# Kernel optimization log

Measured on AMD Instinct MI355X. Metric: run time of the kernel, lower is better.

Reference implementation:

```python
import jax, jax.numpy as jnp
import numpy as np

N = 4096  # input_features == output_features == transform length (power of 2)


def _fft(x, twiddle_factors):
    """Faithful vectorized form of the module's radix-2 butterfly network.

    x: (N, D) complex64. twiddle_factors: (N, D) float32 (the learned weights).
    Original loop: for each stage `step`, for each block, for r in [0, half):
        k = r * (N // step)
        temp = exp(-2j*pi*k/N * twiddle_factors[k]) * x[j + half]
        new x[j + half] = x[j] - temp ; new x[j] = x[j] + temp
    Blocks are independent, so each stage is a single batched butterfly.
    """
    n = x.shape[0]
    # initial permutation: index xor with N//2 (as written in the source; not full bit-reversal)
    x = x[jnp.bitwise_xor(jnp.arange(n), n // 2)]
    step = 2
    while step <= n:  # log2(N) stages, fixed small Python loop
        half = step // 2
        k = jnp.arange(half) * (n // step)                      # (half,)
        phase = (-2.0 * jnp.pi) * (k[:, None].astype(jnp.float32) / n) * twiddle_factors[k]
        tw = jnp.exp(1j * phase)                                # (half, D) complex64
        xr = x.reshape(n // step, step, -1)                     # (blocks, step, D)
        top = xr[:, :half]
        bot = xr[:, half:]
        temp = tw[None] * bot                                   # (blocks, half, D)
        x = jnp.concatenate([top + temp, top - temp], axis=1).reshape(n, -1)
        step *= 2
    return x


def setup_inputs() -> dict:
    key = jax.random.key(0)
    kx, kw = jax.random.split(key)
    x = jax.random.normal(kx, (N, N), dtype=jnp.float32)
    weights = jax.random.normal(kw, (N, N), dtype=jnp.float32)  # nn.Parameter(randn(out, in))
    return {"x": x, "weights": weights}


def reference(x, weights):
    # input_features == output_features -> no pad / no truncation branch taken
    return _fft(x.astype(jnp.complex64), weights)
```

## Files before the change

kernel.cpp:

```cpp
#include <hip/hip_runtime.h>

#define INV_N (1.0f / 4096.0f)

__device__ __forceinline__ void bf(float& ar, float& ai, float& br, float& bi,
                                   float s, float cs) {
    float tr = cs * br - s * bi;
    float ti = cs * bi + s * br;
    br = ar - tr; bi = ai - ti;
    ar = ar + tr; ai = ai + ti;
}

__device__ __forceinline__ void tw(int k, float wk, float* s, float* cs) {
    float rev = (float)k * (-INV_N) * wk;
    rev = __builtin_amdgcn_fractf(rev);
    *s  = __builtin_amdgcn_sinf(rev);
    *cs = __builtin_amdgcn_cosf(rev);
}

__device__ __forceinline__ void exchange(float2* tile, float (&ar)[16],
                                         float (&ai)[16], int pb, int c) {
#pragma unroll
    for (int par = 0; par < 2; ++par) {
#pragma unroll
        for (int m = 0; m < 16; ++m) {
            if (((pb + (m >> 2) + (m & 3)) & 1) == par) {
                int srow = (pb << 3) + (((m >> 2) << 1) | ((m & 3) >> 1));
                tile[srow * 64 + c] = make_float2(ar[m], ai[m]);
            }
        }
        __syncthreads();
#pragma unroll
        for (int m = 0; m < 16; ++m) {
            if (((pb + (m >> 2) + (m & 3)) & 1) == par) {
                int srow = ((m >> 2) << 3) + ((m & 3) << 1) + (pb >> 1);
                float2 v = tile[srow * 64 + c];
                ar[m] = v.x; ai[m] = v.y;
            }
        }
        if (par == 0) __syncthreads();
    }
}

__global__ __launch_bounds__(256) void fft_lo(const float* __restrict__ x,
                                              const float* __restrict__ w,
                                              float2* __restrict__ dst2,
                                              unsigned dst_lim2) {
    __shared__ __align__(16) float2 tile[32 * 64];
    const int t   = threadIdx.x;
    const int c   = t & 63;
    const int pb  = t >> 6;
    const int c0  = (blockIdx.x & 63) << 6;
    const int r0  = (blockIdx.x >> 6) << 6;
    const int src_r0 = r0 ^ 2048;
    const unsigned col = (unsigned)(c0 + c);

    float ar[16], ai[16];
#pragma unroll
    for (int m = 0; m < 16; ++m) {
        unsigned gi = (unsigned)(src_r0 + 16 * pb + m) * 4096u + col;
        ar[m] = __builtin_nontemporal_load(&x[gi]);
        ai[m] = 0.f;
    }

    float wp1[7];
#pragma unroll
    for (int i = 0; i < 7; ++i)
        wp1[i] = w[(unsigned)(256 * (i + 1)) * 4096u + col];

    float w2a[4], w2b[8];
#pragma unroll
    for (int i = 0; i < 4; ++i)
        w2a[i] = w[(unsigned)((pb + 4 * i) * 128) * 4096u + col];
#pragma unroll
    for (int i = 0; i < 8; ++i)
        w2b[i] = w[(unsigned)((pb + 4 * i) * 64) * 4096u + col];

    float s1[8], c1[8];
    s1[0] = 0.f; c1[0] = 1.f;
#pragma unroll
    for (int i = 1; i < 8; ++i)
        tw(256 * i, wp1[i - 1], &s1[i], &c1[i]);

#pragma unroll
    for (int h = 1; h <= 8; h <<= 1) {
        const int step = h << 1;
#pragma unroll
        for (int r = 0; r < h; ++r) {
            const int ti = r * (8 / h);
            const float s = s1[ti], cs = c1[ti];
#pragma unroll
            for (int b = 0; b < 8 / h; ++b) {
                const int mt = b * step + r;
                bf(ar[mt], ai[mt], ar[mt + h], ai[mt + h], s, cs);
            }
        }
    }

    float s2a[4], c2a[4], s2b[8], c2b[8];
#pragma unroll
    for (int i = 0; i < 4; ++i)
        tw((pb + 4 * i) * 128, w2a[i], &s2a[i], &c2a[i]);
#pragma unroll
    for (int i = 0; i < 8; ++i)
        tw((pb + 4 * i) * 64, w2b[i], &s2b[i], &c2b[i]);

    exchange(tile, ar, ai, pb, c);

#pragma unroll
    for (int rm = 0; rm < 4; ++rm) {
#pragma unroll
        for (int b = 0; b < 2; ++b) {
            const int mt = b * 8 + rm;
            bf(ar[mt], ai[mt], ar[mt + 4], ai[mt + 4], s2a[rm], c2a[rm]);
        }
    }
#pragma unroll
    for (int m = 0; m < 8; ++m)
        bf(ar[m], ai[m], ar[m + 8], ai[m + 8], s2b[m], c2b[m]);

#pragma unroll
    for (int m = 0; m < 16; ++m) {
        unsigned gi = (unsigned)(r0 + pb + 4 * m) * 4096u + col;
        if (gi < dst_lim2) dst2[gi] = make_float2(ar[m], ai[m]);
    }
}

template <int REAL_OUT>
__global__ __launch_bounds__(256) void fft_hi(const float* __restrict__ w,
                                              const float2* __restrict__ src2,
                                              float2* __restrict__ dstc,
                                              float* __restrict__ dstr,
                                              unsigned dst_lim) {
    __shared__ __align__(16) float2 tile[32 * 64];
    const int t    = threadIdx.x;
    const int c    = t & 63;
    const int pb   = t >> 6;
    const int rres = blockIdx.x >> 6;
    const unsigned col = (unsigned)(((blockIdx.x & 63) << 6) + c);

    float ar[16], ai[16];
#pragma unroll
    for (int m = 0; m < 16; ++m) {
        unsigned gi = (unsigned)(rres + 64 * (16 * pb + m)) * 4096u + col;
        float2 v = src2[gi];
        ar[m] = v.x; ai[m] = v.y;
    }

    float wp1, wp2[2], wp4[4], wp8[8];
    wp1 = w[(unsigned)(rres * 32) * 4096u + col];
#pragma unroll
    for (int r = 0; r < 2; ++r)
        wp2[r] = w[(unsigned)((rres + 64 * r) * 16) * 4096u + col];
#pragma unroll
    for (int r = 0; r < 4; ++r)
        wp4[r] = w[(unsigned)((rres + 64 * r) * 8) * 4096u + col];
#pragma unroll
    for (int r = 0; r < 8; ++r)
        wp8[r] = w[(unsigned)((rres + 64 * r) * 4) * 4096u + col];

    float w2a[4], w2b[8];
#pragma unroll
    for (int i = 0; i < 4; ++i)
        w2a[i] = w[(unsigned)((rres + 64 * (pb + 4 * i)) * 2) * 4096u + col];
#pragma unroll
    for (int i = 0; i < 8; ++i)
        w2b[i] = w[(unsigned)(rres + 64 * (pb + 4 * i)) * 4096u + col];

    {
        float s, cs;
        tw(rres * 32, wp1, &s, &cs);
#pragma unroll
        for (int b = 0; b < 8; ++b)
            bf(ar[2 * b], ai[2 * b], ar[2 * b + 1], ai[2 * b + 1], s, cs);
    }
#pragma unroll
    for (int r = 0; r < 2; ++r) {
        float s, cs;
        tw((rres + 64 * r) * 16, wp2[r], &s, &cs);
#pragma unroll
        for (int b = 0; b < 4; ++b) {
            const int mt = b * 4 + r;
            bf(ar[mt], ai[mt], ar[mt + 2], ai[mt + 2], s, cs);
        }
    }
#pragma unroll
    for (int r = 0; r < 4; ++r) {
        float s, cs;
        tw((rres + 64 * r) * 8, wp4[r], &s, &cs);
#pragma unroll
        for (int b = 0; b < 2; ++b) {
            const int mt = b * 8 + r;
            bf(ar[mt], ai[mt], ar[mt + 4], ai[mt + 4], s, cs);
        }
    }
#pragma unroll
    for (int r = 0; r < 8; ++r) {
        float s, cs;
        tw((rres + 64 * r) * 4, wp8[r], &s, &cs);
        bf(ar[r], ai[r], ar[r + 8], ai[r + 8], s, cs);
    }

    float s2a[4], c2a[4], s2b[8], c2b[8];
#pragma unroll
    for (int i = 0; i < 4; ++i)
        tw((rres + 64 * (pb + 4 * i)) * 2, w2a[i], &s2a[i], &c2a[i]);
#pragma unroll
    for (int i = 0; i < 8; ++i)
        tw(rres + 64 * (pb + 4 * i), w2b[i], &s2b[i], &c2b[i]);

    exchange(tile, ar, ai, pb, c);

#pragma unroll
    for (int rm = 0; rm < 4; ++rm) {
#pragma unroll
        for (int b = 0; b < 2; ++b) {
            const int mt = b * 8 + rm;
            bf(ar[mt], ai[mt], ar[mt + 4], ai[mt + 4], s2a[rm], c2a[rm]);
        }
    }
#pragma unroll
    for (int m = 0; m < 8; ++m)
        bf(ar[m], ai[m], ar[m + 8], ai[m + 8], s2b[m], c2b[m]);

    if (REAL_OUT) {
#pragma unroll
        for (int m = 0; m < 16; ++m) {
            unsigned gi = (unsigned)(rres + 64 * (pb + 4 * m)) * 4096u + col;
            if (gi < dst_lim) __builtin_nontemporal_store(ar[m], &dstr[gi]);
        }
    } else {
#pragma unroll
        for (int m = 0; m < 16; ++m) {
            unsigned gi = (unsigned)(rres + 64 * (pb + 4 * m)) * 4096u + col;
            if (gi < dst_lim) dstc[gi] = make_float2(ar[m], ai[m]);
        }
    }
}

extern "C" void kernel_launch(void* const* d_in, const int* in_sizes, int n_in,
                              void* d_out, int out_size, void* d_ws, size_t ws_size,
                              hipStream_t stream) {
    const float* x = (const float*)d_in[0];
    const float* w = (const float*)d_in[1];
    const long long NN = 4096LL * 4096LL;

    if ((long long)out_size >= 2 * NN) {
        float2* o2 = (float2*)d_out;
        unsigned lim2 = (unsigned)(out_size / 2);
        fft_lo<<<4096, 256, 0, stream>>>(x, w, o2, lim2);
        fft_hi<0><<<4096, 256, 0, stream>>>(w, o2, o2, nullptr, lim2);
    } else {
        float2* ws2 = (float2*)d_ws;
        unsigned ws_lim2 = (unsigned)(ws_size / 8);
        unsigned out_lim = (unsigned)out_size;
        fft_lo<<<4096, 256, 0, stream>>>(x, w, ws2, ws_lim2);
        fft_hi<1><<<4096, 256, 0, stream>>>(w, (const float2*)ws2, nullptr,
                                            (float*)d_out, out_lim);
    }
}
```

Before: 200.5 us.

## Stage twiddle weights into LDS via async global_load_lds and dedupe loads

Replaces per-thread register loads of the twiddle weights with asynchronous direct-to-LDS loads, spread across the four waves so each weight row is fetched once per block instead of redundantly by every wave. Twiddle computation for the second stage group now runs after the exchange and reads from LDS. Custom barrier macros replace __syncthreads, with explicit vmcnt/lgkmcnt waits. This lowers VGPR pressure and redundant global traffic, but adds LDS use (about 14–16 KB more per block), which may reduce occupancy. Correctness relies on hand-written waitcnt handling.

```diff
diff --git a/kernel.cpp b/kernel.cpp
--- a/kernel.cpp
+++ b/kernel.cpp
@@ -17,6 +17,18 @@
     *cs = __builtin_amdgcn_cosf(rev);
 }
 
+__device__ __forceinline__ void load_lds4(const float* gp, float* lp) {
+    __builtin_amdgcn_global_load_lds(
+        (const __attribute__((address_space(1))) void*)gp,
+        (__attribute__((address_space(3))) void*)lp, 4, 0, 0);
+}
+
+#define BAR() do { asm volatile("s_waitcnt lgkmcnt(0)" ::: "memory"); \
+                   __builtin_amdgcn_s_barrier(); } while (0)
+
+#define STAGE_BAR() do { asm volatile("s_waitcnt vmcnt(0)" ::: "memory"); \
+                         __builtin_amdgcn_s_barrier(); } while (0)
+
 __device__ __forceinline__ void exchange(float2* tile, float (&ar)[16],
                                          float (&ai)[16], int pb, int c) {
 #pragma unroll
@@ -28,7 +40,7 @@
                 tile[srow * 64 + c] = make_float2(ar[m], ai[m]);
             }
         }
-        __syncthreads();
+        BAR();
 #pragma unroll
         for (int m = 0; m < 16; ++m) {
             if (((pb + (m >> 2) + (m & 3)) & 1) == par) {
@@ -37,8 +49,23 @@
                 ar[m] = v.x; ai[m] = v.y;
             }
         }
-        if (par == 0) __syncthreads();
-    }
+        if (par == 0) BAR();
+    }
+}
+
+__device__ __forceinline__ unsigned lo_row(int i) {
+    if (i < 32) return (unsigned)(64 * i);
+    if (i < 48) return (unsigned)((i - 32) * 128);
+    return (unsigned)((i - 47) * 256);
+}
+
+__device__ __forceinline__ unsigned hi_row(int i, int rres) {
+    if (i < 32) return (unsigned)(rres + 64 * i);
+    if (i < 48) return (unsigned)((rres + 64 * (i - 32)) * 2);
+    if (i < 56) return (unsigned)((rres + 64 * (i - 48)) * 4);
+    if (i < 60) return (unsigned)((rres + 64 * (i - 56)) * 8);
+    if (i < 62) return (unsigned)((rres + 64 * (i - 60)) * 16);
+    return (unsigned)(rres * 32);
 }
 
 __global__ __launch_bounds__(256) void fft_lo(const float* __restrict__ x,
@@ -46,14 +73,23 @@
                                               float2* __restrict__ dst2,
                                               unsigned dst_lim2) {
     __shared__ __align__(16) float2 tile[32 * 64];
+    __shared__ __align__(16) float  lds_w[55 * 64];
     const int t   = threadIdx.x;
     const int c   = t & 63;
     const int pb  = t >> 6;
+    const int wv  = t >> 6;
     const int c0  = (blockIdx.x & 63) << 6;
     const int r0  = (blockIdx.x >> 6) << 6;
     const int src_r0 = r0 ^ 2048;
     const unsigned col = (unsigned)(c0 + c);
 
+#pragma unroll
+    for (int ii = 0; ii < 14; ++ii) {
+        int i = 4 * ii + wv;
+        if (i < 55)
+            load_lds4(w + (size_t)lo_row(i) * 4096u + col, lds_w + i * 64);
+    }
+
     float ar[16], ai[16];
 #pragma unroll
     for (int m = 0; m < 16; ++m) {
@@ -62,24 +98,13 @@
         ai[m] = 0.f;
     }
 
-    float wp1[7];
-#pragma unroll
-    for (int i = 0; i < 7; ++i)
-        wp1[i] = w[(unsigned)(256 * (i + 1)) * 4096u + col];
-
-    float w2a[4], w2b[8];
-#pragma unroll
-    for (int i = 0; i < 4; ++i)
-        w2a[i] = w[(unsigned)((pb + 4 * i) * 128) * 4096u + col];
-#pragma unroll
-    for (int i = 0; i < 8; ++i)
-        w2b[i] = w[(unsigned)((pb + 4 * i) * 64) * 4096u + col];
+    STAGE_BAR();
 
     float s1[8], c1[8];
     s1[0] = 0.f; c1[0] = 1.f;
 #pragma unroll
-    for (int i = 1; i < 8; ++i)
-        tw(256 * i, wp1[i - 1], &s1[i], &c1[i]);
+    for (int j = 1; j < 8; ++j)
+        tw(256 * j, lds_w[(47 + j) * 64 + c], &s1[j], &c1[j]);
 
 #pragma unroll
     for (int h = 1; h <= 8; h <<= 1) {
@@ -96,15 +121,15 @@
         }
     }
 
+    exchange(tile, ar, ai, pb, c);
+
     float s2a[4], c2a[4], s2b[8], c2b[8];
 #pragma unroll
     for (int i = 0; i < 4; ++i)
-        tw((pb + 4 * i) * 128, w2a[i], &s2a[i], &c2a[i]);
+        tw((pb + 4 * i) * 128, lds_w[(32 + pb + 4 * i) * 64 + c], &s2a[i], &c2a[i]);
 #pragma unroll
     for (int i = 0; i < 8; ++i)
-        tw((pb + 4 * i) * 64, w2b[i], &s2b[i], &c2b[i]);
-
-    exchange(tile, ar, ai, pb, c);
+        tw((pb + 4 * i) * 64, lds_w[(pb + 4 * i) * 64 + c], &s2b[i], &c2b[i]);
 
 #pragma unroll
     for (int rm = 0; rm < 4; ++rm) {
@@ -132,11 +157,20 @@
                                               float* __restrict__ dstr,
                                               unsigned dst_lim) {
     __shared__ __align__(16) float2 tile[32 * 64];
+    __shared__ __align__(16) float  lds_w[63 * 64];
     const int t    = threadIdx.x;
     const int c    = t & 63;
     const int pb   = t >> 6;
+    const int wv   = t >> 6;
     const int rres = blockIdx.x >> 6;
     const unsigned col = (unsigned)(((blockIdx.x & 63) << 6) + c);
+
+#pragma unroll
+    for (int ii = 0; ii < 16; ++ii) {
+        int i = 4 * ii + wv;
+        if (i < 63)
+            load_lds4(w + (size_t)hi_row(i, rres) * 4096u + col, lds_w + i * 64);
+    }
 
     float ar[16], ai[16];
 #pragma unroll
@@ -146,29 +180,11 @@
         ar[m] = v.x; ai[m] = v.y;
     }
 
-    float wp1, wp2[2], wp4[4], wp8[8];
-    wp1 = w[(unsigned)(rres * 32) * 4096u + col];
-#pragma unroll
-    for (int r = 0; r < 2; ++r)
-        wp2[r] = w[(unsigned)((rres + 64 * r) * 16) * 4096u + col];
-#pragma unroll
-    for (int r = 0; r < 4; ++r)
-        wp4[r] = w[(unsigned)((rres + 64 * r) * 8) * 4096u + col];
-#pragma unroll
-    for (int r = 0; r < 8; ++r)
-        wp8[r] = w[(unsigned)((rres + 64 * r) * 4) * 4096u + col];
-
-    float w2a[4], w2b[8];
-#pragma unroll
-    for (int i = 0; i < 4; ++i)
-        w2a[i] = w[(unsigned)((rres + 64 * (pb + 4 * i)) * 2) * 4096u + col];
-#pragma unroll
-    for (int i = 0; i < 8; ++i)
-        w2b[i] = w[(unsigned)(rres + 64 * (pb + 4 * i)) * 4096u + col];
+    STAGE_BAR();
 
     {
         float s, cs;
-        tw(rres * 32, wp1, &s, &cs);
+        tw(rres * 32, lds_w[62 * 64 + c], &s, &cs);
 #pragma unroll
         for (int b = 0; b < 8; ++b)
             bf(ar[2 * b], ai[2 * b], ar[2 * b + 1], ai[2 * b + 1], s, cs);
@@ -176,7 +192,7 @@
 #pragma unroll
     for (int r = 0; r < 2; ++r) {
         float s, cs;
-        tw((rres + 64 * r) * 16, wp2[r], &s, &cs);
+        tw((rres + 64 * r) * 16, lds_w[(60 + r) * 64 + c], &s, &cs);
 #pragma unroll
         for (int b = 0; b < 4; ++b) {
             const int mt = b * 4 + r;
@@ -186,7 +202,7 @@
 #pragma unroll
     for (int r = 0; r < 4; ++r) {
         float s, cs;
-        tw((rres + 64 * r) * 8, wp4[r], &s, &cs);
+        tw((rres + 64 * r) * 8, lds_w[(56 + r) * 64 + c], &s, &cs);
 #pragma unroll
         for (int b = 0; b < 2; ++b) {
             const int mt = b * 8 + r;
@@ -196,19 +212,21 @@
 #pragma unroll
     for (int r = 0; r < 8; ++r) {
         float s, cs;
-        tw((rres + 64 * r) * 4, wp8[r], &s, &cs);
+        tw((rres + 64 * r) * 4, lds_w[(48 + r) * 64 + c], &s, &cs);
         bf(ar[r], ai[r], ar[r + 8], ai[r + 8], s, cs);
     }
 
+    exchange(tile, ar, ai, pb, c);
+
     float s2a[4], c2a[4], s2b[8], c2b[8];
 #pragma unroll
     for (int i = 0; i < 4; ++i)
-        tw((rres + 64 * (pb + 4 * i)) * 2, w2a[i], &s2a[i], &c2a[i]);
+        tw((rres + 64 * (pb + 4 * i)) * 2, lds_w[(32 + pb + 4 * i) * 64 + c],
+           &s2a[i], &c2a[i]);
 #pragma unroll
     for (int i = 0; i < 8; ++i)
-        tw(rres + 64 * (pb + 4 * i), w2b[i], &s2b[i], &c2b[i]);
-
-    exchange(tile, ar, ai, pb, c);
+        tw(rres + 64 * (pb + 4 * i), lds_w[(pb + 4 * i) * 64 + c],
+           &s2b[i], &c2b[i]);
 
 #pragma unroll
     for (int rm = 0; rm < 4; ++rm) {
```

New measurement: 201.3 us. About the same (+0.4%).
